# Performance work log

Measured on AMD Instinct MI355X. Metric: run time of the kernel, lower is better.

Reference implementation:

```python
import jax, jax.numpy as jnp
import numpy as np

DELTA = -5.0
DECAY = 0.95
EPS = 1e-05


def setup_inputs() -> dict:
    key = jax.random.key(0)
    k1, k2, k3 = jax.random.split(key, 3)
    N, K, D = 16384, 1024, 256
    z = jax.random.normal(k1, (N, D), dtype=jnp.float32)
    centroids = jax.random.normal(k2, (K, D), dtype=jnp.float32)
    ema_w = jax.random.normal(k3, (K, D), dtype=jnp.float32)
    ema_cluster_size = jnp.ones((K,), dtype=jnp.float32)
    return {"z": z, "centroids": centroids, "ema_w": ema_w,
            "ema_cluster_size": ema_cluster_size}


def reference(z, centroids, ema_w, ema_cluster_size):
    # z: [N, D]; centroids/ema_w: [K, D]; ema_cluster_size: [K]
    K = centroids.shape[0]
    # squared L2 distances via ||z||^2 - 2 z.C^T + ||c||^2 (same math as
    # sum((z[:,None,:]-C)**2, -1), without the (N,K,D) intermediate)
    z_sq = jnp.sum(z * z, axis=1, keepdims=True)          # [N, 1]
    c_sq = jnp.sum(centroids * centroids, axis=1)         # [K]
    z_dist = z_sq - 2.0 * (z @ centroids.T) + c_sq        # [N, K]
    gamma = jax.nn.softmax(DELTA * z_dist, axis=1)        # [N, K]
    idx = jnp.argmax(gamma, axis=1)                       # [N] int
    # recons = one_hot(idx) @ centroids == gather
    recons = centroids[idx]                               # [N, D]
    # --- EMA codebook update (training branch), expressed purely ---
    counts = jnp.zeros((K,), dtype=z.dtype).at[idx].add(jnp.ones((), z.dtype))
    new_cs = ema_cluster_size * DECAY + (1.0 - DECAY) * counts
    n = jnp.sum(new_cs)
    new_cs = (new_cs + EPS) / (n + K * EPS) * n
    dw = jax.ops.segment_sum(z, idx, num_segments=K)      # == Idx.T @ z, [K, D]
    new_w = ema_w * DECAY + (1.0 - DECAY) * dw
    new_centroids = new_w / new_cs[:, None]
    # straight-through estimator
    recons = z + jax.lax.stop_gradient(recons - z)
    return recons, gamma, new_centroids
```

## Files before the change

### kernel.cpp

```cpp
#include <hip/hip_runtime.h>
#include <hip/hip_bf16.h>


#define DECAY 0.95f
#define OMD   0.05f
#define EPSV  1e-5f

using f32x4  = __attribute__((ext_vector_type(4))) float;
using bf16x8 = __attribute__((ext_vector_type(8))) __bf16;

typedef __attribute__((address_space(3))) unsigned int       lds_uint;
typedef const __attribute__((address_space(1))) unsigned int glb_uint;

__device__ __forceinline__ void gload16(const void* g, const void* l) {
  __builtin_amdgcn_global_load_lds((glb_uint*)(unsigned long long)g,
                                   (lds_uint*)(unsigned int)(unsigned long long)l,
                                   16, 0, 0);
}

__device__ __forceinline__ unsigned short f2bf(float f) {
  unsigned int u = __float_as_uint(f);
  unsigned int r = (u + 0x7FFFu + ((u >> 16) & 1u)) >> 16;
  return (unsigned short)r;
}
__device__ __forceinline__ float bf2f(unsigned short s) {
  return __uint_as_float(((unsigned int)s) << 16);
}

__global__ __launch_bounds__(256) void zero_ws(float4* __restrict__ p, int n4) {
  const int i = blockIdx.x * 256 + threadIdx.x;
  if (i < n4) p[i] = (float4){0.f, 0.f, 0.f, 0.f};
}

__global__ __launch_bounds__(256) void convert_hilo(const float* __restrict__ src,
                                                    unsigned short* __restrict__ hi,
                                                    unsigned short* __restrict__ lo,
                                                    int total8) {
  const int i = blockIdx.x * 256 + threadIdx.x;
  if (i >= total8) return;
  const float4 a = ((const float4*)src)[2 * i];
  const float4 b = ((const float4*)src)[2 * i + 1];
  float f[8] = {a.x, a.y, a.z, a.w, b.x, b.y, b.z, b.w};
  union { unsigned short u[8]; uint4 v; } H, L;
#pragma unroll
  for (int j = 0; j < 8; ++j) {
    H.u[j] = f2bf(f[j]);
    L.u[j] = f2bf(f[j] - bf2f(H.u[j]));
  }
  ((uint4*)hi)[i] = H.v;
  ((uint4*)lo)[i] = L.v;
}

__global__ __launch_bounds__(64) void csq_kernel(const float* __restrict__ cent,
                                                 float* __restrict__ csq) {
  const int k = blockIdx.x;
  const int t = threadIdx.x;
  const float4 v = ((const float4*)(cent + (size_t)k * 256))[t];
  float s = v.x * v.x + v.y * v.y + v.z * v.z + v.w * v.w;
#pragma unroll
  for (int off = 32; off; off >>= 1) s += __shfl_down(s, off);
  if (t == 0) csq[k] = s;
}

__global__ __launch_bounds__(256, 2) void dist_gemm_mfma(
    const unsigned short* __restrict__ zh, const unsigned short* __restrict__ zl,
    const unsigned short* __restrict__ ch, const unsigned short* __restrict__ cl,
    const float* __restrict__ csq, float* __restrict__ dist) {
  __shared__ unsigned short lds[4][128 * 64];

  const int tid  = threadIdx.x;
  const int lane = tid & 63;
  const int w    = tid >> 6;

  const int bid = blockIdx.x;
  const int lin = (bid & 7) * 128 + (bid >> 3);
  const int m0  = (lin >> 3) * 128;
  const int n0  = (lin & 7) * 128;

  const int wm0 = (w >> 1) * 64;
  const int wn0 = (w & 1) * 64;

  f32x4 acc[4][4];
#pragma unroll
  for (int i = 0; i < 4; ++i)
#pragma unroll
    for (int j = 0; j < 4; ++j) acc[i][j] = (f32x4){0.f, 0.f, 0.f, 0.f};

  const int srow = lane >> 3;
  const int scb  = lane & 7;

  for (int d0 = 0; d0 < 256; d0 += 64) {
    __syncthreads();
#pragma unroll
    for (int j = 0; j < 4; ++j) {
      const int r0    = w * 32 + j * 8;
      const int row   = r0 + srow;
      const int chunk = scb ^ (row & 7);
      const size_t go = (size_t)(d0 + chunk * 8);
      gload16(zh + (size_t)(m0 + row) * 256 + go, &lds[0][r0 * 64]);
      gload16(zl + (size_t)(m0 + row) * 256 + go, &lds[1][r0 * 64]);
      gload16(ch + (size_t)(n0 + row) * 256 + go, &lds[2][r0 * 64]);
      gload16(cl + (size_t)(n0 + row) * 256 + go, &lds[3][r0 * 64]);
    }
    __syncthreads();
#pragma unroll
    for (int s = 0; s < 2; ++s) {
      bf16x8 ah[4], al[4], bh[4], bl[4];
      const int kg = s * 4 + (lane >> 4);
#pragma unroll
      for (int f = 0; f < 4; ++f) {
        const int ra = wm0 + f * 16 + (lane & 15);
        const int ca = kg ^ (ra & 7);
        ah[f] = *(const bf16x8*)&lds[0][ra * 64 + ca * 8];
        al[f] = *(const bf16x8*)&lds[1][ra * 64 + ca * 8];
        const int rb = wn0 + f * 16 + (lane & 15);
        const int cb = kg ^ (rb & 7);
        bh[f] = *(const bf16x8*)&lds[2][rb * 64 + cb * 8];
        bl[f] = *(const bf16x8*)&lds[3][rb * 64 + cb * 8];
      }
#pragma unroll
      for (int fm = 0; fm < 4; ++fm)
#pragma unroll
        for (int fn = 0; fn < 4; ++fn) {
          acc[fm][fn] = __builtin_amdgcn_mfma_f32_16x16x32_bf16(ah[fm], bh[fn], acc[fm][fn], 0, 0, 0);
          acc[fm][fn] = __builtin_amdgcn_mfma_f32_16x16x32_bf16(ah[fm], bl[fn], acc[fm][fn], 0, 0, 0);
          acc[fm][fn] = __builtin_amdgcn_mfma_f32_16x16x32_bf16(al[fm], bh[fn], acc[fm][fn], 0, 0, 0);
        }
    }
  }

#pragma unroll
  for (int fn = 0; fn < 4; ++fn) {
    const int col = n0 + wn0 + fn * 16 + (lane & 15);
    const float cq = csq[col];
#pragma unroll
    for (int fm = 0; fm < 4; ++fm) {
      const int row = m0 + wm0 + fm * 16 + ((lane >> 4) << 2);
#pragma unroll
      for (int r = 0; r < 4; ++r)
        dist[(size_t)(row + r) * 1024 + col] = cq - 2.0f * acc[fm][fn][r];
    }
  }
}

__global__ __launch_bounds__(256) void row_softmax(const float* __restrict__ z,
                                                   const float* __restrict__ cent,
                                                   float* __restrict__ gamma,
                                                   float* __restrict__ recons,
                                                   float* __restrict__ dw,
                                                   float* __restrict__ counts,
                                                   int K) {
  const int n = blockIdx.x;
  const int t = threadIdx.x;
  float* row = gamma + (size_t)n * K;
  const float4 s = ((const float4*)row)[t];

  float mv = s.x; int mi = 4 * t;
  if (s.y < mv) { mv = s.y; mi = 4 * t + 1; }
  if (s.z < mv) { mv = s.z; mi = 4 * t + 2; }
  if (s.w < mv) { mv = s.w; mi = 4 * t + 3; }

#pragma unroll
  for (int off = 32; off; off >>= 1) {
    const float ov = __shfl_down(mv, off);
    const int   oi = __shfl_down(mi, off);
    if (ov < mv || (ov == mv && oi < mi)) { mv = ov; mi = oi; }
  }

  __shared__ float wv[4];
  __shared__ int   wi[4];
  __shared__ float fmin_s;
  __shared__ int   fidx_s;
  __shared__ float fsum_s;
  const int wave = t >> 6;
  if ((t & 63) == 0) { wv[wave] = mv; wi[wave] = mi; }
  __syncthreads();
  if (t == 0) {
    float bv = wv[0]; int bi = wi[0];
#pragma unroll
    for (int wq = 1; wq < 4; ++wq)
      if (wv[wq] < bv || (wv[wq] == bv && wi[wq] < bi)) { bv = wv[wq]; bi = wi[wq]; }
    fmin_s = bv; fidx_s = bi;
  }
  __syncthreads();

  const float bm = fmin_s;
  const float e0 = __expf(-5.0f * (s.x - bm));
  const float e1 = __expf(-5.0f * (s.y - bm));
  const float e2 = __expf(-5.0f * (s.z - bm));
  const float e3 = __expf(-5.0f * (s.w - bm));
  float ls = e0 + e1 + e2 + e3;
#pragma unroll
  for (int off = 32; off; off >>= 1) ls += __shfl_down(ls, off);
  if ((t & 63) == 0) wv[wave] = ls;
  __syncthreads();
  if (t == 0) fsum_s = wv[0] + wv[1] + wv[2] + wv[3];
  __syncthreads();

  const float inv = 1.0f / fsum_s;
  float4 g;
  g.x = e0 * inv; g.y = e1 * inv; g.z = e2 * inv; g.w = e3 * inv;
  ((float4*)row)[t] = g;

  const int idx = fidx_s;
  const float zv = z[(size_t)n * 256 + t];
  recons[(size_t)n * 256 + t] = cent[(size_t)idx * 256 + t];
  atomicAdd(&dw[(size_t)idx * 256 + t], zv);
  if (t == 0) atomicAdd(&counts[idx], 1.0f);
}

__global__ __launch_bounds__(1024) void finalize_cs(const float* __restrict__ ema_cs,
                                                    const float* __restrict__ counts,
                                                    float* __restrict__ newcs, int K) {
  const int t = threadIdx.x;
  const float v = ema_cs[t] * DECAY + OMD * counts[t];
  float sum = v;
#pragma unroll
  for (int off = 32; off; off >>= 1) sum += __shfl_down(sum, off);
  __shared__ float wsum[16];
  __shared__ float tot_s;
  if ((t & 63) == 0) wsum[t >> 6] = sum;
  __syncthreads();
  if (t == 0) {
    float a = 0.0f;
#pragma unroll
    for (int i = 0; i < 16; ++i) a += wsum[i];
    tot_s = a;
  }
  __syncthreads();
  const float n = tot_s;
  newcs[t] = (v + EPSV) / (n + (float)K * EPSV) * n;
}

__global__ __launch_bounds__(256) void finalize_centroids(const float* __restrict__ ema_w,
                                                          const float* __restrict__ dw,
                                                          const float* __restrict__ newcs,
                                                          float* __restrict__ outc,
                                                          int total) {
  const int i = blockIdx.x * 256 + threadIdx.x;
  if (i < total) {
    const int k = i >> 8;
    outc[i] = (ema_w[i] * DECAY + OMD * dw[i]) / newcs[k];
  }
}

extern "C" void kernel_launch(void* const* d_in, const int* in_sizes, int n_in,
                              void* d_out, int out_size, void* d_ws, size_t ws_size,
                              hipStream_t stream) {
  const float* z      = (const float*)d_in[0];
  const float* cent   = (const float*)d_in[1];
  const float* ema_w  = (const float*)d_in[2];
  const float* ema_cs = (const float*)d_in[3];

  const int K = in_sizes[3];
  const int D = in_sizes[1] / K;
  const int N = in_sizes[0] / D;

  float* out    = (float*)d_out;
  float* recons = out;
  float* gamma  = out + (size_t)N * D;
  float* outc   = gamma + (size_t)N * K;

  unsigned short* zh  = (unsigned short*)recons;
  unsigned short* zl  = zh + (size_t)N * D;
  unsigned short* chp = (unsigned short*)outc;
  unsigned short* clp = chp + (size_t)K * D;

  float* dw     = (float*)d_ws;
  float* counts = dw + (size_t)K * D;
  float* csq    = counts + K;
  float* newcs  = csq + K;

  const int n4 = (K * D + K + 3) / 4;
  zero_ws<<<(n4 + 255) / 256, 256, 0, stream>>>((float4*)dw, n4);

  convert_hilo<<<(N * D / 8 + 255) / 256, 256, 0, stream>>>(z, zh, zl, N * D / 8);
  convert_hilo<<<(K * D / 8 + 255) / 256, 256, 0, stream>>>(cent, chp, clp, K * D / 8);

  csq_kernel<<<K, 64, 0, stream>>>(cent, csq);

  dist_gemm_mfma<<<(N / 128) * (K / 128), 256, 0, stream>>>(zh, zl, chp, clp, csq, gamma);

  row_softmax<<<N, 256, 0, stream>>>(z, cent, gamma, recons, dw, counts, K);

  finalize_cs<<<1, K, 0, stream>>>(ema_cs, counts, newcs, K);

  finalize_centroids<<<(K * D + 255) / 256, 256, 0, stream>>>(ema_w, dw, newcs, outc, K * D);
}
```

Baseline: 96.04 us.

## Fuse prep kernels, use one wave per softmax row, merge finalize

Merges the zeroing, centroid hi/lo bf16 conversion and centroid-norm kernels into one prep launch, which also sums ema_cluster_size up front. Because the total of new cluster sizes is then known analytically (DECAY*sum(ema_cs) + OMD*N), the two finalize kernels collapse into one. The row softmax now handles one row per wave with shuffle-only reductions and no block barriers, using float4 loads for the z/centroid gather. This cuts launch count and synchronization, at the cost of relying on counts summing exactly to N.

```diff
diff --git a/kernel.cpp b/kernel.cpp
--- a/kernel.cpp
+++ b/kernel.cpp
@@ -27,9 +27,45 @@
   return __uint_as_float(((unsigned int)s) << 16);
 }
 
-__global__ __launch_bounds__(256) void zero_ws(float4* __restrict__ p, int n4) {
-  const int i = blockIdx.x * 256 + threadIdx.x;
-  if (i < n4) p[i] = (float4){0.f, 0.f, 0.f, 0.f};
+__global__ __launch_bounds__(256) void prep(const float* __restrict__ cent,
+                                            const float* __restrict__ ema_cs,
+                                            unsigned short* __restrict__ chp,
+                                            unsigned short* __restrict__ clp,
+                                            float* __restrict__ csq,
+                                            float* __restrict__ dwzero,
+                                            float* __restrict__ S) {
+  const int bid = blockIdx.x;
+  const int t   = threadIdx.x;
+  if (bid < 128) {
+    const int i = bid * 256 + t;
+    const float4 a = ((const float4*)cent)[2 * i];
+    const float4 b = ((const float4*)cent)[2 * i + 1];
+    float f[8] = {a.x, a.y, a.z, a.w, b.x, b.y, b.z, b.w};
+    union { unsigned short u[8]; uint4 v; } H, L;
+    float ss = 0.f;
+#pragma unroll
+    for (int j = 0; j < 8; ++j) {
+      H.u[j] = f2bf(f[j]);
+      L.u[j] = f2bf(f[j] - bf2f(H.u[j]));
+      ss += f[j] * f[j];
+    }
+    ((uint4*)chp)[i] = H.v;
+    ((uint4*)clp)[i] = L.v;
+#pragma unroll
+    for (int off = 16; off; off >>= 1) ss += __shfl_down(ss, off, 32);
+    if ((t & 31) == 0) csq[bid * 8 + (t >> 5)] = ss;
+  } else if (bid < 385) {
+    const int i = (bid - 128) * 256 + t;
+    ((float4*)dwzero)[i] = (float4){0.f, 0.f, 0.f, 0.f};
+  } else {
+    float s = ema_cs[t] + ema_cs[t + 256] + ema_cs[t + 512] + ema_cs[t + 768];
+#pragma unroll
+    for (int off = 32; off; off >>= 1) s += __shfl_down(s, off);
+    __shared__ float wsum[4];
+    if ((t & 63) == 0) wsum[t >> 6] = s;
+    __syncthreads();
+    if (t == 0) S[0] = wsum[0] + wsum[1] + wsum[2] + wsum[3];
+  }
 }
 
 __global__ __launch_bounds__(256) void convert_hilo(const float* __restrict__ src,
@@ -51,17 +87,6 @@
   ((uint4*)lo)[i] = L.v;
 }
 
-__global__ __launch_bounds__(64) void csq_kernel(const float* __restrict__ cent,
-                                                 float* __restrict__ csq) {
-  const int k = blockIdx.x;
-  const int t = threadIdx.x;
-  const float4 v = ((const float4*)(cent + (size_t)k * 256))[t];
-  float s = v.x * v.x + v.y * v.y + v.z * v.z + v.w * v.w;
-#pragma unroll
-  for (int off = 32; off; off >>= 1) s += __shfl_down(s, off);
-  if (t == 0) csq[k] = s;
-}
-
 __global__ __launch_bounds__(256, 2) void dist_gemm_mfma(
     const unsigned short* __restrict__ zh, const unsigned short* __restrict__ zl,
     const unsigned short* __restrict__ ch, const unsigned short* __restrict__ cl,
@@ -148,100 +173,81 @@
                                                    float* __restrict__ gamma,
                                                    float* __restrict__ recons,
                                                    float* __restrict__ dw,
-                                                   float* __restrict__ counts,
-                                                   int K) {
-  const int n = blockIdx.x;
-  const int t = threadIdx.x;
-  float* row = gamma + (size_t)n * K;
-  const float4 s = ((const float4*)row)[t];
-
-  float mv = s.x; int mi = 4 * t;
-  if (s.y < mv) { mv = s.y; mi = 4 * t + 1; }
-  if (s.z < mv) { mv = s.z; mi = 4 * t + 2; }
-  if (s.w < mv) { mv = s.w; mi = 4 * t + 3; }
-
+                                                   float* __restrict__ counts) {
+  const int wave = threadIdx.x >> 6;
+  const int lane = threadIdx.x & 63;
+  const int n = blockIdx.x * 4 + wave;
+  float* row = gamma + (size_t)n * 1024;
+
+  float4 s4[4];
+  float mv = 3.0e38f; int mi = 0;
+#pragma unroll
+  for (int i = 0; i < 4; ++i) {
+    s4[i] = *(const float4*)&row[i * 256 + lane * 4];
+    const float* f = (const float*)&s4[i];
+#pragma unroll
+    for (int j = 0; j < 4; ++j) {
+      if (f[j] < mv) { mv = f[j]; mi = i * 256 + lane * 4 + j; }
+    }
+  }
 #pragma unroll
   for (int off = 32; off; off >>= 1) {
     const float ov = __shfl_down(mv, off);
     const int   oi = __shfl_down(mi, off);
     if (ov < mv || (ov == mv && oi < mi)) { mv = ov; mi = oi; }
   }
-
-  __shared__ float wv[4];
-  __shared__ int   wi[4];
-  __shared__ float fmin_s;
-  __shared__ int   fidx_s;
-  __shared__ float fsum_s;
-  const int wave = t >> 6;
-  if ((t & 63) == 0) { wv[wave] = mv; wi[wave] = mi; }
-  __syncthreads();
-  if (t == 0) {
-    float bv = wv[0]; int bi = wi[0];
-#pragma unroll
-    for (int wq = 1; wq < 4; ++wq)
-      if (wv[wq] < bv || (wv[wq] == bv && wi[wq] < bi)) { bv = wv[wq]; bi = wi[wq]; }
-    fmin_s = bv; fidx_s = bi;
-  }
-  __syncthreads();
-
-  const float bm = fmin_s;
-  const float e0 = __expf(-5.0f * (s.x - bm));
-  const float e1 = __expf(-5.0f * (s.y - bm));
-  const float e2 = __expf(-5.0f * (s.z - bm));
-  const float e3 = __expf(-5.0f * (s.w - bm));
-  float ls = e0 + e1 + e2 + e3;
-#pragma unroll
-  for (int off = 32; off; off >>= 1) ls += __shfl_down(ls, off);
-  if ((t & 63) == 0) wv[wave] = ls;
-  __syncthreads();
-  if (t == 0) fsum_s = wv[0] + wv[1] + wv[2] + wv[3];
-  __syncthreads();
-
-  const float inv = 1.0f / fsum_s;
-  float4 g;
-  g.x = e0 * inv; g.y = e1 * inv; g.z = e2 * inv; g.w = e3 * inv;
-  ((float4*)row)[t] = g;
-
-  const int idx = fidx_s;
-  const float zv = z[(size_t)n * 256 + t];
-  recons[(size_t)n * 256 + t] = cent[(size_t)idx * 256 + t];
-  atomicAdd(&dw[(size_t)idx * 256 + t], zv);
-  if (t == 0) atomicAdd(&counts[idx], 1.0f);
-}
-
-__global__ __launch_bounds__(1024) void finalize_cs(const float* __restrict__ ema_cs,
-                                                    const float* __restrict__ counts,
-                                                    float* __restrict__ newcs, int K) {
+  mv = __shfl(mv, 0);
+  mi = __shfl(mi, 0);
+
+  float4 e4[4];
+  float ls = 0.f;
+#pragma unroll
+  for (int i = 0; i < 4; ++i) {
+    const float* f = (const float*)&s4[i];
+    float* e = (float*)&e4[i];
+#pragma unroll
+    for (int j = 0; j < 4; ++j) {
+      e[j] = __expf(-5.0f * (f[j] - mv));
+      ls += e[j];
+    }
+  }
+#pragma unroll
+  for (int off = 32; off; off >>= 1) ls += __shfl_xor(ls, off);
+  const float inv = 1.0f / ls;
+
+#pragma unroll
+  for (int i = 0; i < 4; ++i) {
+    float4 g = e4[i];
+    g.x *= inv; g.y *= inv; g.z *= inv; g.w *= inv;
+    *(float4*)&row[i * 256 + lane * 4] = g;
+  }
+
+  const int idx = mi;
+  const float4 zv = *(const float4*)&z[(size_t)n * 256 + lane * 4];
+  const float4 cv = *(const float4*)&cent[(size_t)idx * 256 + lane * 4];
+  *(float4*)&recons[(size_t)n * 256 + lane * 4] = cv;
+  float* dp = &dw[(size_t)idx * 256 + lane * 4];
+  atomicAdd(dp + 0, zv.x);
+  atomicAdd(dp + 1, zv.y);
+  atomicAdd(dp + 2, zv.z);
+  atomicAdd(dp + 3, zv.w);
+  if (lane == 0) atomicAdd(&counts[idx], 1.0f);
+}
+
+__global__ __launch_bounds__(256) void finalize(const float* __restrict__ ema_w,
+                                                const float* __restrict__ ema_cs,
+                                                const float* __restrict__ counts,
+                                                const float* __restrict__ dw,
+                                                const float* __restrict__ S,
+                                                float* __restrict__ outc,
+                                                float fN) {
+  const int k = blockIdx.x;
   const int t = threadIdx.x;
-  const float v = ema_cs[t] * DECAY + OMD * counts[t];
-  float sum = v;
-#pragma unroll
-  for (int off = 32; off; off >>= 1) sum += __shfl_down(sum, off);
-  __shared__ float wsum[16];
-  __shared__ float tot_s;
-  if ((t & 63) == 0) wsum[t >> 6] = sum;
-  __syncthreads();
-  if (t == 0) {
-    float a = 0.0f;
-#pragma unroll
-    for (int i = 0; i < 16; ++i) a += wsum[i];
-    tot_s = a;
-  }
-  __syncthreads();
-  const float n = tot_s;
-  newcs[t] = (v + EPSV) / (n + (float)K * EPSV) * n;
-}
-
-__global__ __launch_bounds__(256) void finalize_centroids(const float* __restrict__ ema_w,
-                                                          const float* __restrict__ dw,
-                                                          const float* __restrict__ newcs,
-                                                          float* __restrict__ outc,
-                                                          int total) {
-  const int i = blockIdx.x * 256 + threadIdx.x;
-  if (i < total) {
-    const int k = i >> 8;
-    outc[i] = (ema_w[i] * DECAY + OMD * dw[i]) / newcs[k];
-  }
+  const float n   = DECAY * S[0] + OMD * fN;
+  const float v   = DECAY * ema_cs[k] + OMD * counts[k];
+  const float ncs = (v + EPSV) / (n + 1024.0f * EPSV) * n;
+  const size_t i  = (size_t)k * 256 + t;
+  outc[i] = (DECAY * ema_w[i] + OMD * dw[i]) / ncs;
 }
 
 extern "C" void kernel_launch(void* const* d_in, const int* in_sizes, int n_in,
@@ -269,21 +275,15 @@
   float* dw     = (float*)d_ws;
   float* counts = dw + (size_t)K * D;
   float* csq    = counts + K;
-  float* newcs  = csq + K;
-
-  const int n4 = (K * D + K + 3) / 4;
-  zero_ws<<<(n4 + 255) / 256, 256, 0, stream>>>((float4*)dw, n4);
+  float* S      = csq + K;
+
+  prep<<<386, 256, 0, stream>>>(cent, ema_cs, chp, clp, csq, dw, S);
 
   convert_hilo<<<(N * D / 8 + 255) / 256, 256, 0, stream>>>(z, zh, zl, N * D / 8);
-  convert_hilo<<<(K * D / 8 + 255) / 256, 256, 0, stream>>>(cent, chp, clp, K * D / 8);
-
-  csq_kernel<<<K, 64, 0, stream>>>(cent, csq);
 
   dist_gemm_mfma<<<(N / 128) * (K / 128), 256, 0, stream>>>(zh, zl, chp, clp, csq, gamma);
 
-  row_softmax<<<N, 256, 0, stream>>>(z, cent, gamma, recons, dw, counts, K);
-
-  finalize_cs<<<1, K, 0, stream>>>(ema_cs, counts, newcs, K);
-
-  finalize_centroids<<<(K * D + 255) / 256, 256, 0, stream>>>(ema_w, dw, newcs, outc, K * D);
-}
+  row_softmax<<<N / 4, 256, 0, stream>>>(z, cent, gamma, recons, dw, counts);
+
+  finalize<<<K, 256, 0, stream>>>(ema_w, ema_cs, counts, dw, S, outc, (float)N);
+}
```

Measured after the change: 179.9 us. +87.3%, slower.
